# Performance work log

Hardware: AMD Instinct MI355X
Metric: run time of the kernel (lower is better)

## Reference

```python
import jax, jax.numpy as jnp
import numpy as np

NUM_GRAPHS = 1024


def setup_inputs() -> dict:
    key = jax.random.key(0)
    k1, k2, k3, k4 = jax.random.split(key, 4)
    N, D = 1000000, 128
    node_embeddings = jax.random.normal(k1, (N, D), dtype=jnp.float32)
    batch_idx = jnp.sort(jax.random.randint(k2, (N,), 0, NUM_GRAPHS))
    # gate MLP params (Linear(D,D) -> ReLU -> Linear(D,1)), scaled like kaiming-ish init
    W1 = jax.random.normal(k3, (D, D), dtype=jnp.float32) / np.sqrt(D)
    b1 = jnp.zeros((D,), dtype=jnp.float32)
    W2 = jax.random.normal(k4, (D, 1), dtype=jnp.float32) / np.sqrt(D)
    b2 = jnp.zeros((1,), dtype=jnp.float32)
    return {"node_embeddings": node_embeddings, "batch_idx": batch_idx,
            "W1": W1, "b1": b1, "W2": W2, "b2": b2}


def reference(node_embeddings, batch_idx, W1, b1, W2, b2):
    # gate = sigmoid(Linear(ReLU(Linear(x))))  -> [N, 1]
    h = jax.nn.relu(node_embeddings @ W1 + b1)          # [N, D]
    gate = jax.nn.sigmoid(h @ W2 + b2)                   # [N, 1]
    gated = gate * node_embeddings                       # [N, D]
    # scatter-sum over batch_idx -> per-graph embedding [B, D]
    graph_embedding = jax.ops.segment_sum(gated, batch_idx, num_segments=NUM_GRAPHS)
    return graph_embedding
```

## Files before the change

### kernel.cpp

```cpp
#include <hip/hip_runtime.h>
#include <stdint.h>

#define D 128
#define TM 64
#define GRID 768
#define NTHREADS 256

typedef float f32x4 __attribute__((ext_vector_type(4)));
typedef short s16x8 __attribute__((ext_vector_type(8)));
typedef uint32_t u32x2 __attribute__((ext_vector_type(2)));

__device__ __forceinline__ uint32_t f2bf_u(float f) {
    union { float f; uint32_t u; } v; v.f = f;
    return (v.u + 0x7fffu + ((v.u >> 16) & 1u)) >> 16;
}
__device__ __forceinline__ short f2bf(float f) { return (short)f2bf_u(f); }
__device__ __forceinline__ float bf2f(uint32_t us) {
    union { uint32_t u; float f; } v; v.u = us << 16; return v.f;
}
__device__ __forceinline__ uint32_t cvt_pk_bf16(float lo, float hi) {
    uint32_t r;
    asm("v_cvt_pk_bf16_f32 %0, %1, %2" : "=v"(r) : "v"(lo), "v"(hi));
    return r;
}

__global__ __launch_bounds__(NTHREADS, 3)
void gate_agg_kernel(const float* __restrict__ X,
                     const int* __restrict__ bidx,
                     const float* __restrict__ W1,
                     const float* __restrict__ b1,
                     const float* __restrict__ W2,
                     const float* __restrict__ b2,
                     float* __restrict__ out,
                     int NT)
{
    __shared__ short w1p[16 * D * 8];
    __shared__ short xtile[TM * D];
    __shared__ float gateL[TM];
    __shared__ int   idxL[TM];

    const int tid = threadIdx.x;
    const int l = tid & 63;
    const int w = tid >> 6;

    for (int i = tid; i < D * D; i += NTHREADS) {
        int k = i >> 7, n = i & 127;
        w1p[(((k >> 3) * D) + n) * 8 + (k & 7)] = f2bf(W1[i]);
    }

    float b1v[8], w2v[8];
    #pragma unroll
    for (int ct = 0; ct < 8; ++ct) {
        b1v[ct] = b1[ct * 16 + (l & 15)];
        w2v[ct] = W2[ct * 16 + (l & 15)];
    }
    const float b2s = b2[0];

    const int q = NT / GRID, rem = NT % GRID;
    int t0, t1;
    if ((int)blockIdx.x < rem) { t0 = blockIdx.x * (q + 1); t1 = t0 + q + 1; }
    else { t0 = rem * (q + 1) + ((int)blockIdx.x - rem) * q; t1 = t0 + q; }

    const int c = tid & 127;
    const int half = tid >> 7;
    float acc3 = 0.0f;
    int cur = -1;

    f32x4 v[8];
    int ridx = 0;
    if (t0 < t1) {
        const float* xg = X + (size_t)t0 * TM * D;
        #pragma unroll
        for (int j = 0; j < 8; ++j)
            v[j] = *(const f32x4*)(xg + (size_t)(j * 256 + tid) * 4);
        if (tid < TM) ridx = bidx[(size_t)t0 * TM + tid];
    }

    __syncthreads();

    for (int t = t0; t < t1; ++t) {
        #pragma unroll
        for (int j = 0; j < 8; ++j) {
            int qc = j * 256 + tid;
            int row = qc >> 5, cq = qc & 31;
            int cc = cq >> 1, h = cq & 1;
            u32x2 wv;
            wv[0] = cvt_pk_bf16(v[j][0], v[j][1]);
            wv[1] = cvt_pk_bf16(v[j][2], v[j][3]);
            *(u32x2*)((char*)xtile + row * 256 + ((cc ^ (row & 15)) << 4) + h * 8) = wv;
        }
        if (tid < TM) idxL[tid] = ridx;
        __syncthreads();

        if (t + 1 < t1) {
            const float* xg = X + (size_t)(t + 1) * TM * D;
            #pragma unroll
            for (int j = 0; j < 8; ++j)
                v[j] = *(const f32x4*)(xg + (size_t)(j * 256 + tid) * 4);
            if (tid < TM) ridx = bidx[(size_t)(t + 1) * TM + tid];
        }

        f32x4 acc[8];
        #pragma unroll
        for (int ct = 0; ct < 8; ++ct) acc[ct] = (f32x4)0.0f;

        const int rowA = w * 16 + (l & 15);
        const char* rbase = (const char*)xtile + rowA * 256;
        #pragma unroll
        for (int kt = 0; kt < 4; ++kt) {
            const int kc = kt * 4 + (l >> 4);
            s16x8 a = *(const s16x8*)(rbase + ((kc ^ (rowA & 15)) << 4));
            #pragma unroll
            for (int ct = 0; ct < 8; ++ct) {
                s16x8 bfr = *(const s16x8*)&w1p[((kt * 4 + (l >> 4)) * D + ct * 16 + (l & 15)) * 8];
                acc[ct] = __builtin_amdgcn_mfma_f32_16x16x32_bf16(a, bfr, acc[ct], 0, 0, 0);
            }
        }

        float p[4] = {0.0f, 0.0f, 0.0f, 0.0f};
        #pragma unroll
        for (int ct = 0; ct < 8; ++ct) {
            #pragma unroll
            for (int r = 0; r < 4; ++r) {
                float h = acc[ct][r] + b1v[ct];
                h = fmaxf(h, 0.0f);
                p[r] = fmaf(h, w2v[ct], p[r]);
            }
        }
        #pragma unroll
        for (int r = 0; r < 4; ++r) {
            #pragma unroll
            for (int m = 1; m < 16; m <<= 1) p[r] += __shfl_xor(p[r], m, 64);
        }
        if ((l & 15) == 0) {
            #pragma unroll
            for (int r = 0; r < 4; ++r) {
                float g = 1.0f / (1.0f + __expf(-(p[r] + b2s)));
                gateL[w * 16 + (l >> 4) * 4 + r] = g;
            }
        }
        __syncthreads();

        #pragma unroll 8
        for (int rr = 0; rr < 32; ++rr) {
            int r = half * 32 + rr;
            int seg = idxL[r];
            float g = gateL[r];
            if (seg != cur) {
                if (cur >= 0) atomicAdd(out + (size_t)cur * D + c, acc3);
                acc3 = 0.0f; cur = seg;
            }
            uint32_t xv = *(const uint16_t*)((const char*)xtile + r * 256 +
                           (((c >> 3) ^ (r & 15)) << 4) + (c & 7) * 2);
            acc3 = fmaf(g, bf2f(xv), acc3);
        }
        __syncthreads();
    }
    if (cur >= 0) atomicAdd(out + (size_t)cur * D + c, acc3);
}

extern "C" void kernel_launch(void* const* d_in, const int* in_sizes, int n_in,
                              void* d_out, int out_size, void* d_ws, size_t ws_size,
                              hipStream_t stream) {
    const float* X    = (const float*)d_in[0];
    const int*   bidx = (const int*)d_in[1];
    const float* W1   = (const float*)d_in[2];
    const float* b1   = (const float*)d_in[3];
    const float* W2   = (const float*)d_in[4];
    const float* b2   = (const float*)d_in[5];
    float* out = (float*)d_out;

    const int N  = in_sizes[0] / D;
    const int NT = N / TM;

    hipMemsetAsync(d_out, 0, (size_t)out_size * sizeof(float), stream);
    gate_agg_kernel<<<GRID, NTHREADS, 0, stream>>>(X, bidx, W1, b1, W2, b2, out, NT);
}
```

Before: 122.0 us.

## Keep W1 fragments in registers and split GEMM columns across waves

W1 is no longer staged in shared memory. Each wave now holds its 32 output columns of W1 as bf16 MFMA fragments in registers and computes all 64 rows for those columns. Each wave writes partial gate dot-products to a padded LDS buffer, and 64 threads sum them and apply the sigmoid. The segment-sum phase now has each thread handle 4 columns over 8 rows using 8-byte LDS loads, which cuts LDS traffic per element but adds a third block barrier and more atomics per segment boundary.

Measured after the change: 122.0 us. Within noise of the previous version (+0.0%).

```diff
diff --git a/kernel.cpp b/kernel.cpp
--- a/kernel.cpp
+++ b/kernel.cpp
@@ -5,6 +5,7 @@
 #define TM 64
 #define GRID 768
 #define NTHREADS 256
+#define PPS 17
 
 typedef float f32x4 __attribute__((ext_vector_type(4)));
 typedef short s16x8 __attribute__((ext_vector_type(8)));
@@ -15,9 +16,6 @@
     return (v.u + 0x7fffu + ((v.u >> 16) & 1u)) >> 16;
 }
 __device__ __forceinline__ short f2bf(float f) { return (short)f2bf_u(f); }
-__device__ __forceinline__ float bf2f(uint32_t us) {
-    union { uint32_t u; float f; } v; v.u = us << 16; return v.f;
-}
 __device__ __forceinline__ uint32_t cvt_pk_bf16(float lo, float hi) {
     uint32_t r;
     asm("v_cvt_pk_bf16_f32 %0, %1, %2" : "=v"(r) : "v"(lo), "v"(hi));
@@ -34,25 +32,33 @@
                      float* __restrict__ out,
                      int NT)
 {
-    __shared__ short w1p[16 * D * 8];
     __shared__ short xtile[TM * D];
-    __shared__ float gateL[TM];
+    __shared__ float pp[64 * PPS];
+    __shared__ u32x2 gidL[TM];
     __shared__ int   idxL[TM];
 
     const int tid = threadIdx.x;
     const int l = tid & 63;
     const int w = tid >> 6;
-
-    for (int i = tid; i < D * D; i += NTHREADS) {
-        int k = i >> 7, n = i & 127;
-        w1p[(((k >> 3) * D) + n) * 8 + (k & 7)] = f2bf(W1[i]);
-    }
-
-    float b1v[8], w2v[8];
+    const int l15 = l & 15;
+    const int lk = l >> 4;
+
+    s16x8 bfr[2][4];
     #pragma unroll
-    for (int ct = 0; ct < 8; ++ct) {
-        b1v[ct] = b1[ct * 16 + (l & 15)];
-        w2v[ct] = W2[ct * 16 + (l & 15)];
+    for (int j = 0; j < 2; ++j) {
+        const int n = (2 * w + j) * 16 + l15;
+        #pragma unroll
+        for (int kt = 0; kt < 4; ++kt) {
+            #pragma unroll
+            for (int e = 0; e < 8; ++e)
+                bfr[j][kt][e] = f2bf(W1[(kt * 32 + lk * 8 + e) * D + n]);
+        }
+    }
+    float b1v[2], w2v[2];
+    #pragma unroll
+    for (int j = 0; j < 2; ++j) {
+        b1v[j] = b1[(2 * w + j) * 16 + l15];
+        w2v[j] = W2[(2 * w + j) * 16 + l15];
     }
     const float b2s = b2[0];
 
@@ -61,9 +67,9 @@
     if ((int)blockIdx.x < rem) { t0 = blockIdx.x * (q + 1); t1 = t0 + q + 1; }
     else { t0 = rem * (q + 1) + ((int)blockIdx.x - rem) * q; t1 = t0 + q; }
 
-    const int c = tid & 127;
-    const int half = tid >> 7;
-    float acc3 = 0.0f;
+    const int cc = tid & 31;
+    const int rg = tid >> 5;
+    float acc3[4] = {0.f, 0.f, 0.f, 0.f};
     int cur = -1;
 
     f32x4 v[8];
@@ -76,18 +82,16 @@
         if (tid < TM) ridx = bidx[(size_t)t0 * TM + tid];
     }
 
-    __syncthreads();
-
     for (int t = t0; t < t1; ++t) {
         #pragma unroll
         for (int j = 0; j < 8; ++j) {
             int qc = j * 256 + tid;
             int row = qc >> 5, cq = qc & 31;
-            int cc = cq >> 1, h = cq & 1;
+            int c2 = cq >> 1, h = cq & 1;
             u32x2 wv;
             wv[0] = cvt_pk_bf16(v[j][0], v[j][1]);
             wv[1] = cvt_pk_bf16(v[j][2], v[j][3]);
-            *(u32x2*)((char*)xtile + row * 256 + ((cc ^ (row & 15)) << 4) + h * 8) = wv;
+            *(u32x2*)((char*)xtile + row * 256 + ((c2 ^ (row & 15)) << 4) + h * 8) = wv;
         }
         if (tid < TM) idxL[tid] = ridx;
         __syncthreads();
@@ -100,63 +104,89 @@
             if (tid < TM) ridx = bidx[(size_t)(t + 1) * TM + tid];
         }
 
-        f32x4 acc[8];
-        #pragma unroll
-        for (int ct = 0; ct < 8; ++ct) acc[ct] = (f32x4)0.0f;
-
-        const int rowA = w * 16 + (l & 15);
-        const char* rbase = (const char*)xtile + rowA * 256;
+        f32x4 acc[4][2];
+        #pragma unroll
+        for (int rf = 0; rf < 4; ++rf) { acc[rf][0] = (f32x4)0.f; acc[rf][1] = (f32x4)0.f; }
+
         #pragma unroll
         for (int kt = 0; kt < 4; ++kt) {
-            const int kc = kt * 4 + (l >> 4);
-            s16x8 a = *(const s16x8*)(rbase + ((kc ^ (rowA & 15)) << 4));
-            #pragma unroll
-            for (int ct = 0; ct < 8; ++ct) {
-                s16x8 bfr = *(const s16x8*)&w1p[((kt * 4 + (l >> 4)) * D + ct * 16 + (l & 15)) * 8];
-                acc[ct] = __builtin_amdgcn_mfma_f32_16x16x32_bf16(a, bfr, acc[ct], 0, 0, 0);
+            const int kc = kt * 4 + lk;
+            #pragma unroll
+            for (int rf = 0; rf < 4; ++rf) {
+                const int R = rf * 16 + l15;
+                s16x8 a = *(const s16x8*)((const char*)xtile + R * 256 + ((kc ^ l15) << 4));
+                acc[rf][0] = __builtin_amdgcn_mfma_f32_16x16x32_bf16(a, bfr[0][kt], acc[rf][0], 0, 0, 0);
+                acc[rf][1] = __builtin_amdgcn_mfma_f32_16x16x32_bf16(a, bfr[1][kt], acc[rf][1], 0, 0, 0);
             }
         }
 
-        float p[4] = {0.0f, 0.0f, 0.0f, 0.0f};
-        #pragma unroll
-        for (int ct = 0; ct < 8; ++ct) {
+        #pragma unroll
+        for (int rf = 0; rf < 4; ++rf) {
+            float pr[4];
             #pragma unroll
             for (int r = 0; r < 4; ++r) {
-                float h = acc[ct][r] + b1v[ct];
-                h = fmaxf(h, 0.0f);
-                p[r] = fmaf(h, w2v[ct], p[r]);
+                float s = 0.f;
+                #pragma unroll
+                for (int j = 0; j < 2; ++j) {
+                    float h = acc[rf][j][r] + b1v[j];
+                    h = fmaxf(h, 0.f);
+                    s = fmaf(h, w2v[j], s);
+                }
+                s += __shfl_xor(s, 1, 64);
+                s += __shfl_xor(s, 2, 64);
+                pr[r] = s;
             }
-        }
-        #pragma unroll
-        for (int r = 0; r < 4; ++r) {
-            #pragma unroll
-            for (int m = 1; m < 16; m <<= 1) p[r] += __shfl_xor(p[r], m, 64);
-        }
-        if ((l & 15) == 0) {
-            #pragma unroll
-            for (int r = 0; r < 4; ++r) {
-                float g = 1.0f / (1.0f + __expf(-(p[r] + b2s)));
-                gateL[w * 16 + (l >> 4) * 4 + r] = g;
+            float val = pr[0];
+            val = ((l & 3) == 1) ? pr[1] : val;
+            val = ((l & 3) == 2) ? pr[2] : val;
+            val = ((l & 3) == 3) ? pr[3] : val;
+            pp[(rf * 16 + lk * 4 + (l & 3)) * PPS + w * 4 + ((l >> 2) & 3)] = val;
+        }
+        __syncthreads();
+
+        if (tid < TM) {
+            float s = 0.f;
+            #pragma unroll
+            for (int c = 0; c < 16; ++c) s += pp[tid * PPS + c];
+            float g = 1.f / (1.f + __expf(-(s + b2s)));
+            u32x2 gi; gi[0] = __float_as_uint(g); gi[1] = (uint32_t)idxL[tid];
+            gidL[tid] = gi;
+        }
+        __syncthreads();
+
+        #pragma unroll
+        for (int rr = 0; rr < 8; ++rr) {
+            int r = rg * 8 + rr;
+            u32x2 gi = gidL[r];
+            int seg = (int)gi[1];
+            float g = __uint_as_float(gi[0]);
+            if (seg != cur) {
+                if (cur >= 0) {
+                    #pragma unroll
+                    for (int i = 0; i < 4; ++i)
+                        atomicAdd(out + (size_t)cur * D + 4 * cc + i, acc3[i]);
+                }
+                acc3[0] = acc3[1] = acc3[2] = acc3[3] = 0.f;
+                cur = seg;
             }
-        }
-        __syncthreads();
-
-        #pragma unroll 8
-        for (int rr = 0; rr < 32; ++rr) {
-            int r = half * 32 + rr;
-            int seg = idxL[r];
-            float g = gateL[r];
-            if (seg != cur) {
-                if (cur >= 0) atomicAdd(out + (size_t)cur * D + c, acc3);
-                acc3 = 0.0f; cur = seg;
-            }
-            uint32_t xv = *(const uint16_t*)((const char*)xtile + r * 256 +
-                           (((c >> 3) ^ (r & 15)) << 4) + (c & 7) * 2);
-            acc3 = fmaf(g, bf2f(xv), acc3);
-        }
-        __syncthreads();
-    }
-    if (cur >= 0) atomicAdd(out + (size_t)cur * D + c, acc3);
+            u32x2 xw = *(const u32x2*)((const char*)xtile + r * 256 +
+                        (((cc >> 1) ^ (r & 15)) << 4) + (cc & 1) * 8);
+            float f0 = __uint_as_float(xw[0] << 16);
+            float f1 = __uint_as_float(xw[0] & 0xffff0000u);
+            float f2 = __uint_as_float(xw[1] << 16);
+            float f3 = __uint_as_float(xw[1] & 0xffff0000u);
+            acc3[0] = fmaf(g, f0, acc3[0]);
+            acc3[1] = fmaf(g, f1, acc3[1]);
+            acc3[2] = fmaf(g, f2, acc3[2]);
+            acc3[3] = fmaf(g, f3, acc3[3]);
+        }
+        __syncthreads();
+    }
+    if (cur >= 0) {
+        #pragma unroll
+        for (int i = 0; i < 4; ++i)
+            atomicAdd(out + (size_t)cur * D + 4 * cc + i, acc3[i]);
+    }
 }
 
 extern "C" void kernel_launch(void* const* d_in, const int* in_sizes, int n_in,
```
